# Performance work log

Measured on AMD Instinct MI355X. Metric: run time of the kernel, lower is better.

Reference implementation:

```python
import jax, jax.numpy as jnp
import numpy as np

CHUNK = 64          # config.memory_chunk_size
MAX_LR = 0.2        # config.max_memory_lr
MIN_DECAY = 0.5     # config.min_memory_decay
MAX_NORM = 30.0     # config.memory_max_norm
NORM_EPS = 1e-5     # config.norm_eps (F.normalize eps)


def setup_inputs() -> dict:
    key = jax.random.key(0)
    k0, k1 = jax.random.split(key)
    B, S, d_in, d_out = 8, 8192, 384, 384
    x = jax.random.normal(k0, (B, S, d_in), dtype=jnp.float32)
    # xavier_uniform with gain=0.1
    bound = 0.1 * float(np.sqrt(6.0 / (d_in + d_out)))
    M_init = jax.random.uniform(k1, (d_out, d_in), minval=-bound, maxval=bound, dtype=jnp.float32)
    eta_raw = jnp.asarray(np.log(0.08 / 0.92), jnp.float32)    # inv_sigmoid(memory_lr_init)
    alpha_raw = jnp.asarray(np.log(0.85 / 0.15), jnp.float32)  # inv_sigmoid(memory_decay_init)
    gate_w = jnp.zeros((1, d_in), jnp.float32)                 # nn.init.zeros_
    gate_b = jnp.full((1,), 2.0, jnp.float32)                  # nn.init.constant_(2.0)
    return {"x": x, "M_init": M_init, "eta_raw": eta_raw, "alpha_raw": alpha_raw,
            "gate_w": gate_w, "gate_b": gate_b}


def reference(x, M_init, eta_raw, alpha_raw, gate_w, gate_b):
    B, S, d_in = x.shape
    d_out = M_init.shape[0]
    eta = jax.nn.sigmoid(eta_raw) * MAX_LR
    alpha = MIN_DECAY + jax.nn.sigmoid(alpha_raw) * (1.0 - MIN_DECAY)

    n_chunks = S // CHUNK  # S chosen divisible by CHUNK => chunk_scale == 1.0
    xc = x.reshape(B, n_chunks, CHUNK, d_in).transpose(1, 0, 2, 3)  # [n,B,C,d_in]
    M0 = jnp.broadcast_to(M_init[None], (B, d_out, d_in)).astype(x.dtype)

    def step(M, chunk):
        # retrieve: queries @ M^T -> [B,C,d_out]
        out = jnp.einsum('bcd,bod->bco', chunk, M)
        # normalize keys (F.normalize: x / max(||x||, eps))
        norms = jnp.linalg.norm(chunk, axis=-1, keepdims=True)
        keys = chunk / jnp.maximum(norms, NORM_EPS)
        k_mean = keys.mean(axis=1)   # [B,d_in]
        v_mean = out.mean(axis=1)    # [B,d_out]
        # delta rule
        Mk = jnp.einsum('bod,bd->bo', M, k_mean)
        err = v_mean - Mk
        update = err[:, :, None] * k_mean[:, None, :]  # outer product [B,d_out,d_in]
        M_new = alpha * M + eta * update
        # memory gate
        gate = jax.nn.sigmoid(k_mean @ gate_w.T + gate_b)[:, :, None]  # [B,1,1]
        M_new = gate * M_new + (1.0 - gate) * M
        # frobenius norm clamp
        M_norm = jnp.linalg.norm(M_new.reshape(B, -1), axis=-1)[:, None, None]
        scale = jnp.minimum(MAX_NORM / (M_norm + 1e-6), 1.0)
        return M_new * scale, out

    M_fin, outs = jax.lax.scan(step, M0, xc)            # outs: [n,B,C,d_out]
    outputs = outs.transpose(1, 0, 2, 3).reshape(B, S, d_out)
    return outputs, M_fin
```

## Files before the change

### kernel.cpp

```cpp
#include <hip/hip_runtime.h>
#include <cmath>

#define BB 8
#define SS 8192
#define DD 384
#define CH 64
#define NC 128

typedef _Float16 h8_t __attribute__((ext_vector_type(8)));
typedef _Float16 h4_t __attribute__((ext_vector_type(4)));
typedef float f32x4 __attribute__((ext_vector_type(4)));

#define MFMA __builtin_amdgcn_mfma_f32_16x16x32_f16

__global__ __launch_bounds__(512) void k1_stats(
    const float* __restrict__ x, const float* __restrict__ M0,
    const float* __restrict__ eta_raw, const float* __restrict__ alpha_raw,
    const float* __restrict__ gate_w, const float* __restrict__ gate_b,
    _Float16* __restrict__ XF, _Float16* __restrict__ UF,
    _Float16* __restrict__ KF, float* __restrict__ AB, float* __restrict__ TAB,
    float* __restrict__ SKK, _Float16* __restrict__ M0H)
{
    __shared__ float ch[CH][DD];
    __shared__ float rinv[CH];
    __shared__ float redg[8], redk[8];
    const int wg = blockIdx.x, tid = threadIdx.x;
    const int b = wg >> 7, n = wg & 127;
    const int lane = tid & 63, wid = tid >> 6;

    if (wg < 64) {
        for (int i = tid; i < 2304; i += 512) {
            int idx = wg * 2304 + i;
            M0H[idx] = (_Float16)M0[idx];
        }
    }

    const size_t chunk_off = (size_t)(b * SS + n * CH) * DD;
    const float4* __restrict__ xin = (const float4*)(x + chunk_off);
    h4_t* __restrict__ xf = (h4_t*)(XF + chunk_off);
    for (int i = tid; i < CH * DD / 4; i += 512) {
        float4 v = xin[i];
        int base = i * 4, r = base / DD, c = base % DD;
        ch[r][c] = v.x; ch[r][c + 1] = v.y; ch[r][c + 2] = v.z; ch[r][c + 3] = v.w;
        h4_t h; h[0] = (_Float16)v.x; h[1] = (_Float16)v.y;
        h[2] = (_Float16)v.z; h[3] = (_Float16)v.w;
        xf[i] = h;
    }
    __syncthreads();

    for (int r = wid * 8; r < wid * 8 + 8; ++r) {
        float s = 0.f;
        for (int t = 0; t < 6; ++t) { float v = ch[r][lane + 64 * t]; s += v * v; }
        for (int off = 32; off; off >>= 1) s += __shfl_xor(s, off);
        if (lane == 0) rinv[r] = 1.f / fmaxf(sqrtf(s), 1e-5f);
    }
    __syncthreads();

    float gpart = 0.f, skkp = 0.f;
    for (int d = tid; d < DD; d += 512) {
        float xa = 0.f, km = 0.f;
        for (int c = 0; c < CH; ++c) { float v = ch[c][d]; xa += v; km += v * rinv[c]; }
        xa *= (1.f / 64.f); km *= (1.f / 64.f);
        int o = (b * NC + n) * DD + d;
        UF[o] = (_Float16)(xa - km);
        KF[o] = (_Float16)km;
        gpart += km * gate_w[d];
        skkp += km * km;
    }
    for (int off = 32; off; off >>= 1) {
        gpart += __shfl_xor(gpart, off);
        skkp += __shfl_xor(skkp, off);
    }
    if (lane == 0) { redg[wid] = gpart; redk[wid] = skkp; }
    __syncthreads();
    if (tid == 0) {
        float gsum = 0.f, ks = 0.f;
        for (int i = 0; i < 8; ++i) { gsum += redg[i]; ks += redk[i]; }
        float g = 1.f / (1.f + expf(-(gsum + gate_b[0])));
        float eta = 0.2f / (1.f + expf(-eta_raw[0]));
        float alpha = 0.5f + 0.5f / (1.f + expf(-alpha_raw[0]));
        float A = g * alpha + 1.f - g;
        float Bc = g * eta;
        AB[wg * 2 + 0] = A;
        AB[wg * 2 + 1] = Bc;
        TAB[wg] = Bc / A;
        SKK[wg] = ks;
    }
}

__global__ __launch_bounds__(256) void k_gram(
    const _Float16* __restrict__ KF, const _Float16* __restrict__ UF,
    const float* __restrict__ TAB, _Float16* __restrict__ GT,
    _Float16* __restrict__ HT)
{
    const int b = blockIdx.x;
    const int tid = threadIdx.x, lane = tid & 63, w = tid >> 6;
    const int q = lane >> 4, l15 = lane & 15;
    const _Float16* Kb = KF + (size_t)b * NC * DD;
    const _Float16* Ub = UF + (size_t)b * NC * DD;
    for (int pass = 0; pass < 2; ++pass) {
        const _Float16* Bm = pass ? Kb : Ub;
        _Float16* Out = pass ? HT : GT;
        f32x4 acc[2][8];
        for (int mt = 0; mt < 2; ++mt)
            for (int nt = 0; nt < 8; ++nt) acc[mt][nt] = (f32x4){0.f, 0.f, 0.f, 0.f};
        for (int kd = 0; kd < 12; ++kd) {
            h8_t af[2];
            for (int mt = 0; mt < 2; ++mt) {
                int j = w * 32 + mt * 16 + l15;
                af[mt] = *(const h8_t*)&Kb[(size_t)j * DD + kd * 32 + q * 8];
            }
            h8_t bf[8];
            for (int nt = 0; nt < 8; ++nt) {
                int nn = nt * 16 + l15;
                bf[nt] = *(const h8_t*)&Bm[(size_t)nn * DD + kd * 32 + q * 8];
            }
            for (int mt = 0; mt < 2; ++mt)
                for (int nt = 0; nt < 8; ++nt)
                    acc[mt][nt] = MFMA(af[mt], bf[nt], acc[mt][nt], 0, 0, 0);
        }
        for (int mt = 0; mt < 2; ++mt)
            for (int nt = 0; nt < 8; ++nt)
                for (int r = 0; r < 4; ++r) {
                    int j = w * 32 + mt * 16 + q * 4 + r;
                    int nn = nt * 16 + l15;
                    float v = (j < nn) ? TAB[b * NC + j] * acc[mt][nt][r] : 0.f;
                    Out[((size_t)b * NC + nn) * NC + j] = (_Float16)v;
                }
    }
}

__global__ __launch_bounds__(256) void k_v0(
    const _Float16* __restrict__ UF, const _Float16* __restrict__ M0H,
    _Float16* __restrict__ V0T)
{
    const int b = blockIdx.x / 3, ob = blockIdx.x % 3;
    const int tid = threadIdx.x, lane = tid & 63, w = tid >> 6;
    const int q = lane >> 4, l15 = lane & 15;
    f32x4 acc[2][8];
    for (int mt = 0; mt < 2; ++mt)
        for (int ot = 0; ot < 8; ++ot) acc[mt][ot] = (f32x4){0.f, 0.f, 0.f, 0.f};
    for (int kd = 0; kd < 12; ++kd) {
        h8_t af[2];
        for (int mt = 0; mt < 2; ++mt) {
            int n = w * 32 + mt * 16 + l15;
            af[mt] = *(const h8_t*)&UF[((size_t)b * NC + n) * DD + kd * 32 + q * 8];
        }
        h8_t bf[8];
        for (int ot = 0; ot < 8; ++ot) {
            int o = ob * 128 + ot * 16 + l15;
            bf[ot] = *(const h8_t*)&M0H[(size_t)o * DD + kd * 32 + q * 8];
        }
        for (int mt = 0; mt < 2; ++mt)
            for (int ot = 0; ot < 8; ++ot)
                acc[mt][ot] = MFMA(af[mt], bf[ot], acc[mt][ot], 0, 0, 0);
    }
    for (int mt = 0; mt < 2; ++mt)
        for (int ot = 0; ot < 8; ++ot)
            for (int r = 0; r < 4; ++r) {
                int n = w * 32 + mt * 16 + q * 4 + r;
                int o = ob * 128 + ot * 16 + l15;
                V0T[((size_t)b * NC + n) * DD + o] = (_Float16)acc[mt][ot][r];
            }
}

__global__ __launch_bounds__(256) void k_chain(
    const _Float16* __restrict__ SRC, const _Float16* __restrict__ V0T,
    const _Float16* __restrict__ GT, _Float16* __restrict__ DST)
{
    __shared__ _Float16 T[128 * 136];
    const int b = blockIdx.x / 3, ob = blockIdx.x % 3;
    const int tid = threadIdx.x, lane = tid & 63, w = tid >> 6;
    const int q = lane >> 4, l15 = lane & 15;
    for (int p = 0; p < 8; ++p) {
        int j = p * 16 + (tid >> 4), o0 = (tid & 15) * 8;
        h8_t v = *(const h8_t*)&SRC[((size_t)b * NC + j) * DD + ob * 128 + o0];
        for (int i = 0; i < 8; ++i) T[(o0 + i) * 136 + j] = v[i];
    }
    __syncthreads();
    f32x4 acc[2][8];
    for (int mt = 0; mt < 2; ++mt)
        for (int ot = 0; ot < 8; ++ot) acc[mt][ot] = (f32x4){0.f, 0.f, 0.f, 0.f};
    for (int kd = 0; kd < 4; ++kd) {
        h8_t af[2];
        for (int mt = 0; mt < 2; ++mt) {
            int n = w * 32 + mt * 16 + l15;
            af[mt] = *(const h8_t*)&GT[((size_t)b * NC + n) * NC + kd * 32 + q * 8];
        }
        h8_t bf[8];
        for (int ot = 0; ot < 8; ++ot)
            bf[ot] = *(const h8_t*)&T[(ot * 16 + l15) * 136 + kd * 32 + q * 8];
        for (int mt = 0; mt < 2; ++mt)
            for (int ot = 0; ot < 8; ++ot)
                acc[mt][ot] = MFMA(af[mt], bf[ot], acc[mt][ot], 0, 0, 0);
    }
    for (int mt = 0; mt < 2; ++mt)
        for (int ot = 0; ot < 8; ++ot)
            for (int r = 0; r < 4; ++r) {
                int n = w * 32 + mt * 16 + q * 4 + r;
                int o = ob * 128 + ot * 16 + l15;
                size_t ix = ((size_t)b * NC + n) * DD + o;
                DST[ix] = (_Float16)((float)V0T[ix] + acc[mt][ot][r]);
            }
}

__global__ __launch_bounds__(256) void k_what(
    const _Float16* __restrict__ KF, const _Float16* __restrict__ M0H,
    const _Float16* __restrict__ HT, const _Float16* __restrict__ VHT,
    float* __restrict__ SVP, float* __restrict__ SVVP)
{
    __shared__ _Float16 T[128 * 136];
    const int b = blockIdx.x / 3, ob = blockIdx.x % 3;
    const int tid = threadIdx.x, lane = tid & 63, w = tid >> 6;
    const int q = lane >> 4, l15 = lane & 15;
    for (int p = 0; p < 8; ++p) {
        int j = p * 16 + (tid >> 4), o0 = (tid & 15) * 8;
        h8_t v = *(const h8_t*)&VHT[((size_t)b * NC + j) * DD + ob * 128 + o0];
        for (int i = 0; i < 8; ++i) T[(o0 + i) * 136 + j] = v[i];
    }
    __syncthreads();
    f32x4 acc[2][8];
    for (int mt = 0; mt < 2; ++mt)
        for (int ot = 0; ot < 8; ++ot) acc[mt][ot] = (f32x4){0.f, 0.f, 0.f, 0.f};
    for (int kd = 0; kd < 12; ++kd) {
        h8_t af[2];
        for (int mt = 0; mt < 2; ++mt) {
            int n = w * 32 + mt * 16 + l15;
            af[mt] = *(const h8_t*)&KF[((size_t)b * NC + n) * DD + kd * 32 + q * 8];
        }
        h8_t bf[8];
        for (int ot = 0; ot < 8; ++ot) {
            int o = ob * 128 + ot * 16 + l15;
            bf[ot] = *(const h8_t*)&M0H[(size_t)o * DD + kd * 32 + q * 8];
        }
        for (int mt = 0; mt < 2; ++mt)
            for (int ot = 0; ot < 8; ++ot)
                acc[mt][ot] = MFMA(af[mt], bf[ot], acc[mt][ot], 0, 0, 0);
    }
    for (int kd = 0; kd < 4; ++kd) {
        h8_t af[2];
        for (int mt = 0; mt < 2; ++mt) {
            int n = w * 32 + mt * 16 + l15;
            af[mt] = *(const h8_t*)&HT[((size_t)b * NC + n) * NC + kd * 32 + q * 8];
        }
        h8_t bf[8];
        for (int ot = 0; ot < 8; ++ot)
            bf[ot] = *(const h8_t*)&T[(ot * 16 + l15) * 136 + kd * 32 + q * 8];
        for (int mt = 0; mt < 2; ++mt)
            for (int ot = 0; ot < 8; ++ot)
                acc[mt][ot] = MFMA(af[mt], bf[ot], acc[mt][ot], 0, 0, 0);
    }
    for (int mt = 0; mt < 2; ++mt)
        for (int r = 0; r < 4; ++r) {
            int n = w * 32 + mt * 16 + q * 4 + r;
            float sv = 0.f, svv = 0.f;
            for (int ot = 0; ot < 8; ++ot) {
                float vh = (float)T[(ot * 16 + l15) * 136 + n];
                sv += acc[mt][ot][r] * vh;
                svv += vh * vh;
            }
            sv += __shfl_xor(sv, 1); svv += __shfl_xor(svv, 1);
            sv += __shfl_xor(sv, 2); svv += __shfl_xor(svv, 2);
            sv += __shfl_xor(sv, 4); svv += __shfl_xor(svv, 4);
            sv += __shfl_xor(sv, 8); svv += __shfl_xor(svv, 8);
            if (l15 == 0) {
                SVP[(b * 3 + ob) * NC + n] = sv;
                SVVP[(b * 3 + ob) * NC + n] = svv;
            }
        }
}

__global__ __launch_bounds__(256) void k_scalar(
    const float* __restrict__ M0, const float* __restrict__ AB,
    const float* __restrict__ SKK, const float* __restrict__ SVP,
    const float* __restrict__ SVVP, float* __restrict__ SIG,
    float* __restrict__ FRHO)
{
    const int b = blockIdx.x, tid = threadIdx.x;
    __shared__ float red[4];
    __shared__ float sig_s[NC];
    float p = 0.f;
    const float4* m4 = (const float4*)M0;
    for (int i = tid; i < DD * DD / 4; i += 256) {
        float4 v = m4[i];
        p += v.x * v.x + v.y * v.y + v.z * v.z + v.w * v.w;
    }
    for (int off = 32; off; off >>= 1) p += __shfl_xor(p, off);
    if ((tid & 63) == 0) red[tid >> 6] = p;
    __syncthreads();
    if (tid == 0) {
        float phi2 = red[0] + red[1] + red[2] + red[3];
        float an = 1.f, rho = 1.f;
        for (int n = 0; n < NC; ++n) {
            float A = AB[(b * NC + n) * 2], Bc = AB[(b * NC + n) * 2 + 1];
            sig_s[n] = rho * an;
            float a2 = an * an;
            float sv = a2 * (SVP[(b * 3 + 0) * NC + n] + SVP[(b * 3 + 1) * NC + n]
                             + SVP[(b * 3 + 2) * NC + n]);
            float svv = a2 * (SVVP[(b * 3 + 0) * NC + n] + SVVP[(b * 3 + 1) * NC + n]
                              + SVVP[(b * 3 + 2) * NC + n]);
            phi2 = A * A * phi2 + 2.f * A * Bc * sv + Bc * Bc * svv * SKK[b * NC + n];
            float s = fminf(30.f / (rho * sqrtf(phi2) + 1e-6f), 1.f);
            rho *= s; an *= A;
        }
        FRHO[b] = rho * an;
    }
    __syncthreads();
    for (int i = tid; i < NC; i += 256) SIG[b * NC + i] = sig_s[i];
}

__global__ __launch_bounds__(256) void k_trans(
    const _Float16* __restrict__ VHT, const _Float16* __restrict__ KF,
    const float* __restrict__ TAB, _Float16* __restrict__ WTH,
    _Float16* __restrict__ KFT)
{
    __shared__ _Float16 T[128 * 72];
    const int b = blockIdx.x / 6, ob = blockIdx.x % 6, tid = threadIdx.x;
    for (int pass = 0; pass < 2; ++pass) {
        const _Float16* Src = pass ? KF : VHT;
        _Float16* Dst = pass ? KFT : WTH;
        if (pass) __syncthreads();
        for (int pp = 0; pp < 4; ++pp) {
            int j = pp * 32 + (tid >> 3), oo = (tid & 7) * 8;
            *(h8_t*)&T[j * 72 + oo] =
                *(const h8_t*)&Src[((size_t)b * NC + j) * DD + ob * 64 + oo];
        }
        __syncthreads();
        for (int c = 0; c < 4; ++c) {
            int idx = c * 256 + tid;
            int ol = idx >> 4, jc = (idx & 15) * 8;
            h8_t v;
            for (int i = 0; i < 8; ++i) {
                float t = (float)T[(jc + i) * 72 + ol];
                if (!pass) t *= TAB[b * NC + jc + i];
                v[i] = (_Float16)t;
            }
            *(h8_t*)&Dst[((size_t)b * DD + ob * 64 + ol) * NC + jc] = v;
        }
    }
}

__global__ __launch_bounds__(256) void k4_out(
    const _Float16* __restrict__ XF, const _Float16* __restrict__ M0H,
    const _Float16* __restrict__ KF, const _Float16* __restrict__ WTH,
    const _Float16* __restrict__ KFT, const float* __restrict__ SIG,
    const float* __restrict__ FRHO, const float* __restrict__ M0,
    float* __restrict__ out)
{
    const int tid = threadIdx.x, lane = tid & 63, w = tid >> 6;
    const int q = lane >> 4, l15 = lane & 15;

    if (blockIdx.x >= BB * NC) {
        const int tw = blockIdx.x - BB * NC;
        const int b = tw / 12, sub = tw % 12;
        const int obk = sub >> 1, dh = sub & 1;
        const int o_t = obk * 64 + w * 16;
        f32x4 acc[12];
        for (int dt = 0; dt < 12; ++dt) acc[dt] = (f32x4){0.f, 0.f, 0.f, 0.f};
        for (int kd = 0; kd < 4; ++kd) {
            h8_t af = *(const h8_t*)&WTH[((size_t)b * DD + o_t + l15) * NC + kd * 32 + q * 8];
            for (int dt = 0; dt < 12; ++dt) {
                int d = dh * 192 + dt * 16 + l15;
                h8_t bf = *(const h8_t*)&KFT[((size_t)b * DD + d) * NC + kd * 32 + q * 8];
                acc[dt] = MFMA(af, bf, acc[dt], 0, 0, 0);
            }
        }
        float fr = FRHO[b];
        float* dst = out + (size_t)BB * SS * DD;
        for (int dt = 0; dt < 12; ++dt)
            for (int r = 0; r < 4; ++r) {
                int o = o_t + q * 4 + r, d = dh * 192 + dt * 16 + l15;
                dst[((size_t)b * DD + o) * DD + d] =
                    fr * (M0[(size_t)o * DD + d] + acc[dt][r]);
            }
        return;
    }

    const int b = blockIdx.x >> 7, n = blockIdx.x & 127;
    __shared__ _Float16 lds[CH * 392];

    const size_t chunk_off = (size_t)(b * SS + n * CH) * DD;
    {
        const h4_t* __restrict__ xs = (const h4_t*)(XF + chunk_off);
        for (int i = tid; i < CH * DD / 4; i += 256) {
            int base = i * 4, r = base / DD, c = base % DD;
            *(h4_t*)&lds[r * 392 + c] = xs[i];
        }
    }
    __syncthreads();

    f32x4 acc[4][6];
    for (int mi = 0; mi < 4; ++mi)
        for (int nj = 0; nj < 6; ++nj) acc[mi][nj] = (f32x4){0.f, 0.f, 0.f, 0.f};

    for (int kd = 0; kd < 12; ++kd) {
        h8_t af[4];
        for (int mi = 0; mi < 4; ++mi)
            af[mi] = *(const h8_t*)&lds[(mi * 16 + l15) * 392 + kd * 32 + q * 8];
        h8_t bf[6];
        for (int nj = 0; nj < 6; ++nj) {
            int o = w * 96 + nj * 16 + l15;
            bf[nj] = *(const h8_t*)&M0H[(size_t)o * DD + kd * 32 + q * 8];
        }
        for (int mi = 0; mi < 4; ++mi)
            for (int nj = 0; nj < 6; ++nj)
                acc[mi][nj] = MFMA(af[mi], bf[nj], acc[mi][nj], 0, 0, 0);
    }

    const int nb = (n + 31) >> 5;
    const bool sact = (w * 32 < n);
    f32x4 sacc[4][2];
    if (sact) {
        for (int mi = 0; mi < 4; ++mi)
            for (int nj = 0; nj < 2; ++nj) sacc[mi][nj] = (f32x4){0.f, 0.f, 0.f, 0.f};
        for (int kd = 0; kd < 12; ++kd) {
            h8_t af[4];
            for (int mi = 0; mi < 4; ++mi)
                af[mi] = *(const h8_t*)&lds[(mi * 16 + l15) * 392 + kd * 32 + q * 8];
            h8_t bf[2];
            for (int nj = 0; nj < 2; ++nj) {
                int j = w * 32 + nj * 16 + l15;
                bf[nj] = *(const h8_t*)&KF[((size_t)(b * NC) + j) * DD + kd * 32 + q * 8];
            }
            for (int mi = 0; mi < 4; ++mi)
                for (int nj = 0; nj < 2; ++nj)
                    sacc[mi][nj] = MFMA(af[mi], bf[nj], sacc[mi][nj], 0, 0, 0);
        }
    }
    __syncthreads();
    if (sact) {
        for (int mi = 0; mi < 4; ++mi)
            for (int nj = 0; nj < 2; ++nj)
                for (int r = 0; r < 4; ++r) {
                    int c = mi * 16 + q * 4 + r, j = w * 32 + nj * 16 + l15;
                    lds[c * 136 + j] = (_Float16)((j < n) ? sacc[mi][nj][r] : 0.f);
                }
    }
    __syncthreads();

    for (int kb = 0; kb < nb; ++kb) {
        h8_t af[4];
        for (int mi = 0; mi < 4; ++mi)
            af[mi] = *(const h8_t*)&lds[(mi * 16 + l15) * 136 + kb * 32 + q * 8];
        h8_t bf[6];
        for (int nj = 0; nj < 6; ++nj) {
            int o = w * 96 + nj * 16 + l15;
            bf[nj] = *(const h8_t*)&WTH[((size_t)(b * DD) + o) * NC + kb * 32 + q * 8];
        }
        for (int mi = 0; mi < 4; ++mi)
            for (int nj = 0; nj < 6; ++nj)
                acc[mi][nj] = MFMA(af[mi], bf[nj], acc[mi][nj], 0, 0, 0);
    }

    const float sg = SIG[b * NC + n];
    for (int mi = 0; mi < 4; ++mi)
        for (int nj = 0; nj < 6; ++nj)
            for (int r = 0; r < 4; ++r) {
                int c = mi * 16 + q * 4 + r, o = w * 96 + nj * 16 + l15;
                out[chunk_off + (size_t)c * DD + o] = sg * acc[mi][nj][r];
            }
}

extern "C" void kernel_launch(void* const* d_in, const int* in_sizes, int n_in,
                              void* d_out, int out_size, void* d_ws, size_t ws_size,
                              hipStream_t stream) {
    (void)in_sizes; (void)n_in; (void)out_size; (void)ws_size;
    const float* x         = (const float*)d_in[0];
    const float* M0        = (const float*)d_in[1];
    const float* eta_raw   = (const float*)d_in[2];
    const float* alpha_raw = (const float*)d_in[3];
    const float* gate_w    = (const float*)d_in[4];
    const float* gate_b    = (const float*)d_in[5];
    float* out = (float*)d_out;
    char* ws = (char*)d_ws;

    _Float16* XF  = (_Float16*)(ws);
    _Float16* UF  = (_Float16*)(ws + 50331648);
    _Float16* KF  = (_Float16*)(ws + 51118080);
    _Float16* M0H = (_Float16*)(ws + 51904512);
    _Float16* GT  = (_Float16*)(ws + 52199424);
    _Float16* HT  = (_Float16*)(ws + 52461568);
    _Float16* V0T = (_Float16*)(ws + 52723712);
    _Float16* VTA = (_Float16*)(ws + 53510144);
    _Float16* VTB = (_Float16*)(ws + 54296576);
    _Float16* WTH = (_Float16*)(ws + 55083008);
    _Float16* KFT = (_Float16*)(ws + 55869440);
    float*    AB  = (float*)(ws + 56655872);
    float*    TAB = (float*)(ws + 56664064);
    float*    SKK = (float*)(ws + 56668160);
    float*    SVP = (float*)(ws + 56672256);
    float*    SVVP= (float*)(ws + 56684544);
    float*    SIG = (float*)(ws + 56696832);
    float*    FRHO= (float*)(ws + 56700928);

    k1_stats<<<dim3(BB * NC), dim3(512), 0, stream>>>(
        x, M0, eta_raw, alpha_raw, gate_w, gate_b, XF, UF, KF, AB, TAB, SKK, M0H);
    k_gram<<<dim3(BB), dim3(256), 0, stream>>>(KF, UF, TAB, GT, HT);
    k_v0<<<dim3(BB * 3), dim3(256), 0, stream>>>(UF, M0H, V0T);
    k_chain<<<dim3(BB * 3), dim3(256), 0, stream>>>(V0T, V0T, GT, VTA);
    k_chain<<<dim3(BB * 3), dim3(256), 0, stream>>>(VTA, V0T, GT, VTB);
    k_what<<<dim3(BB * 3), dim3(256), 0, stream>>>(KF, M0H, HT, VTB, SVP, SVVP);
    k_scalar<<<dim3(BB), dim3(256), 0, stream>>>(M0, AB, SKK, SVP, SVVP, SIG, FRHO);
    k_trans<<<dim3(BB * 6), dim3(256), 0, stream>>>(VTB, KF, TAB, WTH, KFT);
    k4_out<<<dim3(BB * NC + 96), dim3(256), 0, stream>>>(
        XF, M0H, KF, WTH, KFT, SIG, FRHO, M0, out);
}
```

Before: 492.4 us.

## Split intra-chunk score GEMM into own kernel and merge small launches

Moves the causal score GEMM (chunk queries against earlier chunk keys) out of the output kernel into a separate k_score kernel. That kernel writes fp16 scores to a new workspace buffer, which k4_out then reads straight from global memory instead of staging X in LDS. k_gram with k_v0, and k_scalar with k_trans, are each merged into one launch, the scalar recurrence preloads its inputs into shared memory, and k1_stats keeps its chunk in fp16 in LDS. The aim is to cut launches and LDS pressure so k4_out gets more occupancy (launch bounds 3), at the cost of about 16 MB of extra score traffic through global memory.

```diff
diff --git a/kernel.cpp b/kernel.cpp
--- a/kernel.cpp
+++ b/kernel.cpp
@@ -21,7 +21,7 @@
     _Float16* __restrict__ KF, float* __restrict__ AB, float* __restrict__ TAB,
     float* __restrict__ SKK, _Float16* __restrict__ M0H)
 {
-    __shared__ float ch[CH][DD];
+    __shared__ _Float16 ch[CH * 392];
     __shared__ float rinv[CH];
     __shared__ float redg[8], redk[8];
     const int wg = blockIdx.x, tid = threadIdx.x;
@@ -41,16 +41,18 @@
     for (int i = tid; i < CH * DD / 4; i += 512) {
         float4 v = xin[i];
         int base = i * 4, r = base / DD, c = base % DD;
-        ch[r][c] = v.x; ch[r][c + 1] = v.y; ch[r][c + 2] = v.z; ch[r][c + 3] = v.w;
         h4_t h; h[0] = (_Float16)v.x; h[1] = (_Float16)v.y;
         h[2] = (_Float16)v.z; h[3] = (_Float16)v.w;
+        *(h4_t*)&ch[r * 392 + c] = h;
         xf[i] = h;
     }
     __syncthreads();
 
     for (int r = wid * 8; r < wid * 8 + 8; ++r) {
         float s = 0.f;
-        for (int t = 0; t < 6; ++t) { float v = ch[r][lane + 64 * t]; s += v * v; }
+        for (int t = 0; t < 6; ++t) {
+            float v = (float)ch[r * 392 + lane + 64 * t]; s += v * v;
+        }
         for (int off = 32; off; off >>= 1) s += __shfl_xor(s, off);
         if (lane == 0) rinv[r] = 1.f / fmaxf(sqrtf(s), 1e-5f);
     }
@@ -59,7 +61,9 @@
     float gpart = 0.f, skkp = 0.f;
     for (int d = tid; d < DD; d += 512) {
         float xa = 0.f, km = 0.f;
-        for (int c = 0; c < CH; ++c) { float v = ch[c][d]; xa += v; km += v * rinv[c]; }
+        for (int c = 0; c < CH; ++c) {
+            float v = (float)ch[c * 392 + d]; xa += v; km += v * rinv[c];
+        }
         xa *= (1.f / 64.f); km *= (1.f / 64.f);
         int o = (b * NC + n) * DD + d;
         UF[o] = (_Float16)(xa - km);
@@ -88,80 +92,111 @@
     }
 }
 
-__global__ __launch_bounds__(256) void k_gram(
-    const _Float16* __restrict__ KF, const _Float16* __restrict__ UF,
-    const float* __restrict__ TAB, _Float16* __restrict__ GT,
-    _Float16* __restrict__ HT)
-{
-    const int b = blockIdx.x;
+__global__ __launch_bounds__(256) void k_score(
+    const _Float16* __restrict__ XF, const _Float16* __restrict__ KF,
+    _Float16* __restrict__ SG)
+{
+    const int b = blockIdx.x >> 7, n = blockIdx.x & 127;
     const int tid = threadIdx.x, lane = tid & 63, w = tid >> 6;
     const int q = lane >> 4, l15 = lane & 15;
-    const _Float16* Kb = KF + (size_t)b * NC * DD;
-    const _Float16* Ub = UF + (size_t)b * NC * DD;
-    for (int pass = 0; pass < 2; ++pass) {
-        const _Float16* Bm = pass ? Kb : Ub;
-        _Float16* Out = pass ? HT : GT;
+    if (w * 32 >= n) return;
+    const size_t chunk_off = (size_t)(b * SS + n * CH) * DD;
+    f32x4 acc[4][2];
+    for (int mi = 0; mi < 4; ++mi)
+        for (int nj = 0; nj < 2; ++nj) acc[mi][nj] = (f32x4){0.f, 0.f, 0.f, 0.f};
+    for (int kd = 0; kd < 12; ++kd) {
+        h8_t af[4];
+        for (int mi = 0; mi < 4; ++mi)
+            af[mi] = *(const h8_t*)&XF[chunk_off + (size_t)(mi * 16 + l15) * DD + kd * 32 + q * 8];
+        h8_t bf[2];
+        for (int nj = 0; nj < 2; ++nj) {
+            int j = w * 32 + nj * 16 + l15;
+            bf[nj] = *(const h8_t*)&KF[((size_t)b * NC + j) * DD + kd * 32 + q * 8];
+        }
+        for (int mi = 0; mi < 4; ++mi)
+            for (int nj = 0; nj < 2; ++nj)
+                acc[mi][nj] = MFMA(af[mi], bf[nj], acc[mi][nj], 0, 0, 0);
+    }
+    _Float16* Sout = SG + ((size_t)(b * NC + n)) * CH * NC;
+    for (int mi = 0; mi < 4; ++mi)
+        for (int nj = 0; nj < 2; ++nj)
+            for (int r = 0; r < 4; ++r) {
+                int c = mi * 16 + q * 4 + r, j = w * 32 + nj * 16 + l15;
+                Sout[c * NC + j] = (_Float16)((j < n) ? acc[mi][nj][r] : 0.f);
+            }
+}
+
+__global__ __launch_bounds__(256) void kA(
+    const _Float16* __restrict__ KF, const _Float16* __restrict__ UF,
+    const _Float16* __restrict__ M0H, const float* __restrict__ TAB,
+    _Float16* __restrict__ GT, _Float16* __restrict__ HT,
+    _Float16* __restrict__ V0T)
+{
+    const int tid = threadIdx.x, lane = tid & 63, w = tid >> 6;
+    const int q = lane >> 4, l15 = lane & 15;
+    if (blockIdx.x < 8) {
+        const int b = blockIdx.x;
+        const _Float16* Kb = KF + (size_t)b * NC * DD;
+        const _Float16* Ub = UF + (size_t)b * NC * DD;
+        for (int pass = 0; pass < 2; ++pass) {
+            const _Float16* Bm = pass ? Kb : Ub;
+            _Float16* Out = pass ? HT : GT;
+            f32x4 acc[2][8];
+            for (int mt = 0; mt < 2; ++mt)
+                for (int nt = 0; nt < 8; ++nt) acc[mt][nt] = (f32x4){0.f, 0.f, 0.f, 0.f};
+            for (int kd = 0; kd < 12; ++kd) {
+                h8_t af[2];
+                for (int mt = 0; mt < 2; ++mt) {
+                    int j = w * 32 + mt * 16 + l15;
+                    af[mt] = *(const h8_t*)&Kb[(size_t)j * DD + kd * 32 + q * 8];
+                }
+                h8_t bf[8];
+                for (int nt = 0; nt < 8; ++nt) {
+                    int nn = nt * 16 + l15;
+                    bf[nt] = *(const h8_t*)&Bm[(size_t)nn * DD + kd * 32 + q * 8];
+                }
+                for (int mt = 0; mt < 2; ++mt)
+                    for (int nt = 0; nt < 8; ++nt)
+                        acc[mt][nt] = MFMA(af[mt], bf[nt], acc[mt][nt], 0, 0, 0);
+            }
+            for (int mt = 0; mt < 2; ++mt)
+                for (int nt = 0; nt < 8; ++nt)
+                    for (int r = 0; r < 4; ++r) {
+                        int j = w * 32 + mt * 16 + q * 4 + r;
+                        int nn = nt * 16 + l15;
+                        float v = (j < nn) ? TAB[b * NC + j] * acc[mt][nt][r] : 0.f;
+                        Out[((size_t)b * NC + nn) * NC + j] = (_Float16)v;
+                    }
+        }
+    } else {
+        const int idx = blockIdx.x - 8;
+        const int b = idx / 3, ob = idx % 3;
         f32x4 acc[2][8];
         for (int mt = 0; mt < 2; ++mt)
-            for (int nt = 0; nt < 8; ++nt) acc[mt][nt] = (f32x4){0.f, 0.f, 0.f, 0.f};
+            for (int ot = 0; ot < 8; ++ot) acc[mt][ot] = (f32x4){0.f, 0.f, 0.f, 0.f};
         for (int kd = 0; kd < 12; ++kd) {
             h8_t af[2];
             for (int mt = 0; mt < 2; ++mt) {
-                int j = w * 32 + mt * 16 + l15;
-                af[mt] = *(const h8_t*)&Kb[(size_t)j * DD + kd * 32 + q * 8];
+                int n = w * 32 + mt * 16 + l15;
+                af[mt] = *(const h8_t*)&UF[((size_t)b * NC + n) * DD + kd * 32 + q * 8];
             }
             h8_t bf[8];
-            for (int nt = 0; nt < 8; ++nt) {
-                int nn = nt * 16 + l15;
-                bf[nt] = *(const h8_t*)&Bm[(size_t)nn * DD + kd * 32 + q * 8];
+            for (int ot = 0; ot < 8; ++ot) {
+                int o = ob * 128 + ot * 16 + l15;
+                bf[ot] = *(const h8_t*)&M0H[(size_t)o * DD + kd * 32 + q * 8];
             }
             for (int mt = 0; mt < 2; ++mt)
-                for (int nt = 0; nt < 8; ++nt)
-                    acc[mt][nt] = MFMA(af[mt], bf[nt], acc[mt][nt], 0, 0, 0);
-        }
-        for (int mt = 0; mt < 2; ++mt)
-            for (int nt = 0; nt < 8; ++nt)
-                for (int r = 0; r < 4; ++r) {
-                    int j = w * 32 + mt * 16 + q * 4 + r;
-                    int nn = nt * 16 + l15;
-                    float v = (j < nn) ? TAB[b * NC + j] * acc[mt][nt][r] : 0.f;
-                    Out[((size_t)b * NC + nn) * NC + j] = (_Float16)v;
-                }
-    }
-}
-
-__global__ __launch_bounds__(256) void k_v0(
-    const _Float16* __restrict__ UF, const _Float16* __restrict__ M0H,
-    _Float16* __restrict__ V0T)
-{
-    const int b = blockIdx.x / 3, ob = blockIdx.x % 3;
-    const int tid = threadIdx.x, lane = tid & 63, w = tid >> 6;
-    const int q = lane >> 4, l15 = lane & 15;
-    f32x4 acc[2][8];
-    for (int mt = 0; mt < 2; ++mt)
-        for (int ot = 0; ot < 8; ++ot) acc[mt][ot] = (f32x4){0.f, 0.f, 0.f, 0.f};
-    for (int kd = 0; kd < 12; ++kd) {
-        h8_t af[2];
-        for (int mt = 0; mt < 2; ++mt) {
-            int n = w * 32 + mt * 16 + l15;
-            af[mt] = *(const h8_t*)&UF[((size_t)b * NC + n) * DD + kd * 32 + q * 8];
-        }
-        h8_t bf[8];
-        for (int ot = 0; ot < 8; ++ot) {
-            int o = ob * 128 + ot * 16 + l15;
-            bf[ot] = *(const h8_t*)&M0H[(size_t)o * DD + kd * 32 + q * 8];
+                for (int ot = 0; ot < 8; ++ot)
+                    acc[mt][ot] = MFMA(af[mt], bf[ot], acc[mt][ot], 0, 0, 0);
         }
         for (int mt = 0; mt < 2; ++mt)
             for (int ot = 0; ot < 8; ++ot)
-                acc[mt][ot] = MFMA(af[mt], bf[ot], acc[mt][ot], 0, 0, 0);
-    }
-    for (int mt = 0; mt < 2; ++mt)
-        for (int ot = 0; ot < 8; ++ot)
-            for (int r = 0; r < 4; ++r) {
-                int n = w * 32 + mt * 16 + q * 4 + r;
-                int o = ob * 128 + ot * 16 + l15;
-                V0T[((size_t)b * NC + n) * DD + o] = (_Float16)acc[mt][ot][r];
-            }
+                for (int r = 0; r < 4; ++r) {
+                    int n = w * 32 + mt * 16 + q * 4 + r;
+                    int o = ob * 128 + ot * 16 + l15;
+                    V0T[((size_t)b * NC + n) * DD + o] = (_Float16)acc[mt][ot][r];
+                }
+    }
 }
 
 __global__ __launch_bounds__(256) void k_chain(
@@ -270,79 +305,84 @@
         }
 }
 
-__global__ __launch_bounds__(256) void k_scalar(
-    const float* __restrict__ M0, const float* __restrict__ AB,
-    const float* __restrict__ SKK, const float* __restrict__ SVP,
-    const float* __restrict__ SVVP, float* __restrict__ SIG,
-    float* __restrict__ FRHO)
-{
-    const int b = blockIdx.x, tid = threadIdx.x;
-    __shared__ float red[4];
-    __shared__ float sig_s[NC];
-    float p = 0.f;
-    const float4* m4 = (const float4*)M0;
-    for (int i = tid; i < DD * DD / 4; i += 256) {
-        float4 v = m4[i];
-        p += v.x * v.x + v.y * v.y + v.z * v.z + v.w * v.w;
-    }
-    for (int off = 32; off; off >>= 1) p += __shfl_xor(p, off);
-    if ((tid & 63) == 0) red[tid >> 6] = p;
-    __syncthreads();
-    if (tid == 0) {
-        float phi2 = red[0] + red[1] + red[2] + red[3];
-        float an = 1.f, rho = 1.f;
-        for (int n = 0; n < NC; ++n) {
-            float A = AB[(b * NC + n) * 2], Bc = AB[(b * NC + n) * 2 + 1];
-            sig_s[n] = rho * an;
-            float a2 = an * an;
-            float sv = a2 * (SVP[(b * 3 + 0) * NC + n] + SVP[(b * 3 + 1) * NC + n]
-                             + SVP[(b * 3 + 2) * NC + n]);
-            float svv = a2 * (SVVP[(b * 3 + 0) * NC + n] + SVVP[(b * 3 + 1) * NC + n]
-                              + SVVP[(b * 3 + 2) * NC + n]);
-            phi2 = A * A * phi2 + 2.f * A * Bc * sv + Bc * Bc * svv * SKK[b * NC + n];
-            float s = fminf(30.f / (rho * sqrtf(phi2) + 1e-6f), 1.f);
-            rho *= s; an *= A;
-        }
-        FRHO[b] = rho * an;
-    }
-    __syncthreads();
-    for (int i = tid; i < NC; i += 256) SIG[b * NC + i] = sig_s[i];
-}
-
-__global__ __launch_bounds__(256) void k_trans(
+__global__ __launch_bounds__(256) void kC(
     const _Float16* __restrict__ VHT, const _Float16* __restrict__ KF,
-    const float* __restrict__ TAB, _Float16* __restrict__ WTH,
-    _Float16* __restrict__ KFT)
-{
-    __shared__ _Float16 T[128 * 72];
-    const int b = blockIdx.x / 6, ob = blockIdx.x % 6, tid = threadIdx.x;
-    for (int pass = 0; pass < 2; ++pass) {
-        const _Float16* Src = pass ? KF : VHT;
-        _Float16* Dst = pass ? KFT : WTH;
-        if (pass) __syncthreads();
-        for (int pp = 0; pp < 4; ++pp) {
-            int j = pp * 32 + (tid >> 3), oo = (tid & 7) * 8;
-            *(h8_t*)&T[j * 72 + oo] =
-                *(const h8_t*)&Src[((size_t)b * NC + j) * DD + ob * 64 + oo];
-        }
+    const float* __restrict__ TAB, const float* __restrict__ M0,
+    const float* __restrict__ AB, const float* __restrict__ SKK,
+    const float* __restrict__ SVP, const float* __restrict__ SVVP,
+    _Float16* __restrict__ WTH, _Float16* __restrict__ KFT,
+    float* __restrict__ SIG, float* __restrict__ FRHO)
+{
+    const int tid = threadIdx.x;
+    if (blockIdx.x < 48) {
+        __shared__ _Float16 T[128 * 72];
+        const int b = blockIdx.x / 6, ob = blockIdx.x % 6;
+        for (int pass = 0; pass < 2; ++pass) {
+            const _Float16* Src = pass ? KF : VHT;
+            _Float16* Dst = pass ? KFT : WTH;
+            if (pass) __syncthreads();
+            for (int pp = 0; pp < 4; ++pp) {
+                int j = pp * 32 + (tid >> 3), oo = (tid & 7) * 8;
+                *(h8_t*)&T[j * 72 + oo] =
+                    *(const h8_t*)&Src[((size_t)b * NC + j) * DD + ob * 64 + oo];
+            }
+            __syncthreads();
+            for (int c = 0; c < 4; ++c) {
+                int idx = c * 256 + tid;
+                int ol = idx >> 4, jc = (idx & 15) * 8;
+                h8_t v;
+                for (int i = 0; i < 8; ++i) {
+                    float t = (float)T[(jc + i) * 72 + ol];
+                    if (!pass) t *= TAB[b * NC + jc + i];
+                    v[i] = (_Float16)t;
+                }
+                *(h8_t*)&Dst[((size_t)b * DD + ob * 64 + ol) * NC + jc] = v;
+            }
+        }
+    } else {
+        __shared__ float sA[NC], sB[NC], sSV[NC], sVV[NC], sKK[NC], sig_s[NC];
+        __shared__ float red[4];
+        const int b = blockIdx.x - 48;
+        for (int i = tid; i < NC; i += 256) {
+            sA[i] = AB[(b * NC + i) * 2];
+            sB[i] = AB[(b * NC + i) * 2 + 1];
+            sSV[i] = SVP[(b * 3 + 0) * NC + i] + SVP[(b * 3 + 1) * NC + i]
+                     + SVP[(b * 3 + 2) * NC + i];
+            sVV[i] = SVVP[(b * 3 + 0) * NC + i] + SVVP[(b * 3 + 1) * NC + i]
+                     + SVVP[(b * 3 + 2) * NC + i];
+            sKK[i] = SKK[b * NC + i];
+        }
+        float p = 0.f;
+        const float4* m4 = (const float4*)M0;
+        for (int i = tid; i < DD * DD / 4; i += 256) {
+            float4 v = m4[i];
+            p += v.x * v.x + v.y * v.y + v.z * v.z + v.w * v.w;
+        }
+        for (int off = 32; off; off >>= 1) p += __shfl_xor(p, off);
+        if ((tid & 63) == 0) red[tid >> 6] = p;
         __syncthreads();
-        for (int c = 0; c < 4; ++c) {
-            int idx = c * 256 + tid;
-            int ol = idx >> 4, jc = (idx & 15) * 8;
-            h8_t v;
-            for (int i = 0; i < 8; ++i) {
-                float t = (float)T[(jc + i) * 72 + ol];
-                if (!pass) t *= TAB[b * NC + jc + i];
-                v[i] = (_Float16)t;
-            }
-            *(h8_t*)&Dst[((size_t)b * DD + ob * 64 + ol) * NC + jc] = v;
-        }
-    }
-}
-
-__global__ __launch_bounds__(256) void k4_out(
+        if (tid == 0) {
+            float phi2 = red[0] + red[1] + red[2] + red[3];
+            float an = 1.f, rho = 1.f;
+            for (int n = 0; n < NC; ++n) {
+                float A = sA[n], Bc = sB[n];
+                sig_s[n] = rho * an;
+                float a2 = an * an;
+                phi2 = A * A * phi2 + 2.f * A * Bc * a2 * sSV[n]
+                       + Bc * Bc * a2 * sVV[n] * sKK[n];
+                float s = fminf(30.f / (rho * sqrtf(phi2) + 1e-6f), 1.f);
+                rho *= s; an *= A;
+            }
+            FRHO[b] = rho * an;
+        }
+        __syncthreads();
+        for (int i = tid; i < NC; i += 256) SIG[b * NC + i] = sig_s[i];
+    }
+}
+
+__global__ __launch_bounds__(256, 3) void k4_out(
     const _Float16* __restrict__ XF, const _Float16* __restrict__ M0H,
-    const _Float16* __restrict__ KF, const _Float16* __restrict__ WTH,
+    const _Float16* __restrict__ SG, const _Float16* __restrict__ WTH,
     const _Float16* __restrict__ KFT, const float* __restrict__ SIG,
     const float* __restrict__ FRHO, const float* __restrict__ M0,
     float* __restrict__ out)
@@ -377,26 +417,16 @@
     }
 
     const int b = blockIdx.x >> 7, n = blockIdx.x & 127;
-    __shared__ _Float16 lds[CH * 392];
-
     const size_t chunk_off = (size_t)(b * SS + n * CH) * DD;
-    {
-        const h4_t* __restrict__ xs = (const h4_t*)(XF + chunk_off);
-        for (int i = tid; i < CH * DD / 4; i += 256) {
-            int base = i * 4, r = base / DD, c = base % DD;
-            *(h4_t*)&lds[r * 392 + c] = xs[i];
-        }
-    }
-    __syncthreads();
-
     f32x4 acc[4][6];
     for (int mi = 0; mi < 4; ++mi)
         for (int nj = 0; nj < 6; ++nj) acc[mi][nj] = (f32x4){0.f, 0.f, 0.f, 0.f};
 
+    const _Float16* __restrict__ Arow = XF + chunk_off;
     for (int kd = 0; kd < 12; ++kd) {
         h8_t af[4];
         for (int mi = 0; mi < 4; ++mi)
-            af[mi] = *(const h8_t*)&lds[(mi * 16 + l15) * 392 + kd * 32 + q * 8];
+            af[mi] = *(const h8_t*)&Arow[(size_t)(mi * 16 + l15) * DD + kd * 32 + q * 8];
         h8_t bf[6];
         for (int nj = 0; nj < 6; ++nj) {
             int o = w * 96 + nj * 16 + l15;
@@ -408,44 +438,15 @@
     }
 
     const int nb = (n + 31) >> 5;
-    const bool sact = (w * 32 < n);
-    f32x4 sacc[4][2];
-    if (sact) {
-        for (int mi = 0; mi < 4; ++mi)
-            for (int nj = 0; nj < 2; ++nj) sacc[mi][nj] = (f32x4){0.f, 0.f, 0.f, 0.f};
-        for (int kd = 0; kd < 12; ++kd) {
-            h8_t af[4];
-            for (int mi = 0; mi < 4; ++mi)
-                af[mi] = *(const h8_t*)&lds[(mi * 16 + l15) * 392 + kd * 32 + q * 8];
-            h8_t bf[2];
-            for (int nj = 0; nj < 2; ++nj) {
-                int j = w * 32 + nj * 16 + l15;
-                bf[nj] = *(const h8_t*)&KF[((size_t)(b * NC) + j) * DD + kd * 32 + q * 8];
-            }
-            for (int mi = 0; mi < 4; ++mi)
-                for (int nj = 0; nj < 2; ++nj)
-                    sacc[mi][nj] = MFMA(af[mi], bf[nj], sacc[mi][nj], 0, 0, 0);
-        }
-    }
-    __syncthreads();
-    if (sact) {
-        for (int mi = 0; mi < 4; ++mi)
-            for (int nj = 0; nj < 2; ++nj)
-                for (int r = 0; r < 4; ++r) {
-                    int c = mi * 16 + q * 4 + r, j = w * 32 + nj * 16 + l15;
-                    lds[c * 136 + j] = (_Float16)((j < n) ? sacc[mi][nj][r] : 0.f);
-                }
-    }
-    __syncthreads();
-
+    const _Float16* __restrict__ Srow = SG + ((size_t)(b * NC + n)) * CH * NC;
     for (int kb = 0; kb < nb; ++kb) {
         h8_t af[4];
         for (int mi = 0; mi < 4; ++mi)
-            af[mi] = *(const h8_t*)&lds[(mi * 16 + l15) * 136 + kb * 32 + q * 8];
+            af[mi] = *(const h8_t*)&Srow[(mi * 16 + l15) * NC + kb * 32 + q * 8];
         h8_t bf[6];
         for (int nj = 0; nj < 6; ++nj) {
             int o = w * 96 + nj * 16 + l15;
-            bf[nj] = *(const h8_t*)&WTH[((size_t)(b * DD) + o) * NC + kb * 32 + q * 8];
+            bf[nj] = *(const h8_t*)&WTH[((size_t)b * DD + o) * NC + kb * 32 + q * 8];
         }
         for (int mi = 0; mi < 4; ++mi)
             for (int nj = 0; nj < 6; ++nj)
@@ -485,23 +486,24 @@
     _Float16* VTB = (_Float16*)(ws + 54296576);
     _Float16* WTH = (_Float16*)(ws + 55083008);
     _Float16* KFT = (_Float16*)(ws + 55869440);
-    float*    AB  = (float*)(ws + 56655872);
-    float*    TAB = (float*)(ws + 56664064);
-    float*    SKK = (float*)(ws + 56668160);
-    float*    SVP = (float*)(ws + 56672256);
-    float*    SVVP= (float*)(ws + 56684544);
-    float*    SIG = (float*)(ws + 56696832);
-    float*    FRHO= (float*)(ws + 56700928);
+    _Float16* SG  = (_Float16*)(ws + 56655872);
+    float*    AB  = (float*)(ws + 73433088);
+    float*    TAB = (float*)(ws + 73441280);
+    float*    SKK = (float*)(ws + 73445376);
+    float*    SVP = (float*)(ws + 73449472);
+    float*    SVVP= (float*)(ws + 73461760);
+    float*    SIG = (float*)(ws + 73474048);
+    float*    FRHO= (float*)(ws + 73478144);
 
     k1_stats<<<dim3(BB * NC), dim3(512), 0, stream>>>(
         x, M0, eta_raw, alpha_raw, gate_w, gate_b, XF, UF, KF, AB, TAB, SKK, M0H);
-    k_gram<<<dim3(BB), dim3(256), 0, stream>>>(KF, UF, TAB, GT, HT);
-    k_v0<<<dim3(BB * 3), dim3(256), 0, stream>>>(UF, M0H, V0T);
+    k_score<<<dim3(BB * NC), dim3(256), 0, stream>>>(XF, KF, SG);
+    kA<<<dim3(8 + BB * 3), dim3(256), 0, stream>>>(KF, UF, M0H, TAB, GT, HT, V0T);
     k_chain<<<dim3(BB * 3), dim3(256), 0, stream>>>(V0T, V0T, GT, VTA);
     k_chain<<<dim3(BB * 3), dim3(256), 0, stream>>>(VTA, V0T, GT, VTB);
     k_what<<<dim3(BB * 3), dim3(256), 0, stream>>>(KF, M0H, HT, VTB, SVP, SVVP);
-    k_scalar<<<dim3(BB), dim3(256), 0, stream>>>(M0, AB, SKK, SVP, SVVP, SIG, FRHO);
-    k_trans<<<dim3(BB * 6), dim3(256), 0, stream>>>(VTB, KF, TAB, WTH, KFT);
+    kC<<<dim3(56), dim3(256), 0, stream>>>(
+        VTB, KF, TAB, M0, AB, SKK, SVP, SVVP, WTH, KFT, SIG, FRHO);
     k4_out<<<dim3(BB * NC + 96), dim3(256), 0, stream>>>(
-        XF, M0H, KF, WTH, KFT, SIG, FRHO, M0, out);
-}
+        XF, M0H, SG, WTH, KFT, SIG, FRHO, M0, out);
+}
```

New measurement: 489.6 us. Within noise of the previous version (-0.6%).
